# Kernel optimization log

Measured on AMD Instinct MI355X. Metric: run time of the kernel, lower is better.

The kernel has to match this reference:

```python
import jax, jax.numpy as jnp
import numpy as np

TAU = 2.0
V_TH = 1.0
ALPHA = 2.0  # ATan surrogate alpha (spikingjelly default)

@jax.custom_vjp
def atan_heaviside(x):
    # Forward: Heaviside spike; backward: ATan surrogate gradient.
    return (x >= 0).astype(x.dtype)

def _atan_fwd(x):
    return atan_heaviside(x), x

def _atan_bwd(x, g):
    sg = (ALPHA / 2.0) / (1.0 + (jnp.pi / 2.0 * ALPHA * x) ** 2)
    return (g * sg,)

atan_heaviside.defvjp(_atan_fwd, _atan_bwd)

def lif_scan(cur):
    # cur: [T, B, F] input currents. LIF: H = V + (X - V)/tau; S = H >= v_th; hard reset V = H*(1-S).
    def step(v, x_t):
        h = v + (x_t - v) / TAU
        s = atan_heaviside(h - V_TH)
        v_new = h * (1.0 - s)
        return v_new, s
    v0 = jnp.zeros(cur.shape[1:], dtype=cur.dtype)
    _, spikes = jax.lax.scan(step, v0, cur)
    return spikes

def setup_inputs() -> dict:
    key = jax.random.key(0)
    k1, k2 = jax.random.split(key)
    T, B, F_in, F_out = 64, 256, 1024, 1024
    x = jax.random.normal(k1, (T, B, F_in), dtype=jnp.float32)
    W = jax.random.normal(k2, (F_out, F_in), dtype=jnp.float32) * (1.0 / np.sqrt(F_in))
    return {"x": x, "W": W}

def reference(x, W):
    # Linear projection over all timesteps, then multi-step LIF recurrence.
    cur = jnp.einsum('tbf,of->tbo', x, W)  # [T, B, F_out]
    return lif_scan(cur)
```

## Files before the change

kernel.cpp:

```cpp
#include <hip/hip_runtime.h>


#define T_DIM 64
#define B_DIM 256
#define F_DIM 1024
#define K_DIM 1024
#define M_DIM 16384
#define COLS  (B_DIM * F_DIM)
#define KP    2048
#define MARGIN 6e-5f
#define LIST_CAP 32768

typedef __attribute__((ext_vector_type(8))) short short8;
typedef __attribute__((ext_vector_type(4))) float floatx4;

#define ASYNC_CP16(gp, lp)                                                     \
    __builtin_amdgcn_global_load_lds(                                          \
        (const __attribute__((address_space(1))) unsigned int*)(gp),           \
        (__attribute__((address_space(3))) unsigned int*)(lp), 16, 0, 0)

#define HARD_SYNC() do {                                                       \
        __builtin_amdgcn_sched_barrier(0);                                     \
        asm volatile("s_waitcnt vmcnt(0) lgkmcnt(0)" ::: "memory");            \
        __syncthreads();                                                       \
        __builtin_amdgcn_sched_barrier(0);                                     \
    } while (0)

__device__ inline unsigned short f32_to_bf16_rne(float f) {
    unsigned int u = __builtin_bit_cast(unsigned int, f);
    unsigned int r = (u + 0x7FFFu + ((u >> 16) & 1u)) >> 16;
    return (unsigned short)r;
}
__device__ inline float bf16_to_f32(unsigned short h) {
    unsigned int u = ((unsigned int)h) << 16;
    return __builtin_bit_cast(float, u);
}

__global__ __launch_bounds__(256) void split_kernel(
    const float* __restrict__ x, const float* __restrict__ Wm,
    unsigned short* __restrict__ A, unsigned short* __restrict__ B,
    unsigned int* __restrict__ counter)
{
    if (blockIdx.x == 0 && threadIdx.x == 0) *counter = 0;
    const int blk = blockIdx.x;
    const float* in;
    unsigned short* dst;
    int g2;
    int orow;
    if (blk < 8192) {
        g2 = blk * 256 + threadIdx.x;
        int e = g2 * 8;
        int row = e >> 10;
        orow = ((row & 255) << 6) | (row >> 8);
        in = x; dst = A;
    } else {
        g2 = (blk - 8192) * 256 + threadIdx.x;
        int e = g2 * 8;
        orow = e >> 10;
        in = Wm; dst = B;
    }
    const int k = (g2 * 8) & 1023;
    float4 v0 = reinterpret_cast<const float4*>(in)[g2 * 2];
    float4 v1 = reinterpret_cast<const float4*>(in)[g2 * 2 + 1];
    float fs[8] = {v0.x, v0.y, v0.z, v0.w, v1.x, v1.y, v1.z, v1.w};
    short8 hv, lv;
#pragma unroll
    for (int i = 0; i < 8; ++i) {
        unsigned short h = f32_to_bf16_rne(fs[i]);
        unsigned short l = f32_to_bf16_rne(fs[i] - bf16_to_f32(h));
        hv[i] = (short)h;
        lv[i] = (short)l;
    }
    reinterpret_cast<short8*>(dst)[(size_t)orow * (KP / 8) + (k >> 3)] = hv;
    reinterpret_cast<short8*>(dst)[(size_t)orow * (KP / 8) + 128 + (k >> 3)] = lv;
}

__global__ __launch_bounds__(512, 2) void gemm_scan_kernel(
    const unsigned short* __restrict__ A,
    const unsigned short* __restrict__ B,
    float* __restrict__ out,
    unsigned int* __restrict__ counter, unsigned int* __restrict__ list)
{
    __shared__ unsigned short Ah0[256 * 32], Al0[256 * 32];
    __shared__ unsigned short Bh0[256 * 32], Bl0[256 * 32];
    __shared__ unsigned short Ah1[256 * 32], Al1[256 * 32];
    __shared__ unsigned short Bh1[256 * 32], Bl1[256 * 32];

    const int tid  = threadIdx.x;
    const int lane = tid & 63;
    const int wv   = tid >> 6;
    const int lid = blockIdx.x;
    const int mt  = ((lid & 7) << 3) | (lid >> 5);
    const int nt  = (lid >> 3) & 3;
    const int m0  = mt * 256;
    const int n0  = nt * 256;
    const int wm  = (wv & 1) * 128;
    const int wn  = (wv >> 1) * 64;

    floatx4 acc[8][4] = {};

    const int srow = tid >> 2;
    const int slin = (tid & 3) * 8;
    const int ssw  = (((tid & 3) ^ ((srow >> 1) & 3)) * 8);
    const int lrow = lane & 15;
    const int q    = lane >> 4;
    const int rsw  = (lrow >> 1) & 3;
    const int sl   = (q ^ rsw) * 8;

    const size_t RKP = (size_t)128 * KP;
    const unsigned short* ga_h = A + (size_t)(m0 + srow) * KP + ssw;
    const unsigned short* ga_l = ga_h + 1024;
    const unsigned short* gb_h = B + (size_t)(n0 + srow) * KP + ssw;
    const unsigned short* gb_l = gb_h + 1024;

    const int ldsA  = srow * 32 + slin;
    const int ldsA2 = (srow + 128) * 32 + slin;

    int aoff[8], boff[4];
#pragma unroll
    for (int i = 0; i < 8; ++i) aoff[i] = (wm + i * 16 + lrow) * 32 + sl;
#pragma unroll
    for (int j = 0; j < 4; ++j) boff[j] = (wn + j * 16 + lrow) * 32 + sl;

#define STAGE(AhB, AlB, BhB, BlB, kk) do {                                     \
        ASYNC_CP16(ga_h + (kk),       &AhB[ldsA]);                             \
        ASYNC_CP16(ga_h + RKP + (kk), &AhB[ldsA2]);                            \
        ASYNC_CP16(ga_l + (kk),       &AlB[ldsA]);                             \
        ASYNC_CP16(ga_l + RKP + (kk), &AlB[ldsA2]);                            \
        ASYNC_CP16(gb_h + (kk),       &BhB[ldsA]);                             \
        ASYNC_CP16(gb_h + RKP + (kk), &BhB[ldsA2]);                            \
        ASYNC_CP16(gb_l + (kk),       &BlB[ldsA]);                             \
        ASYNC_CP16(gb_l + RKP + (kk), &BlB[ldsA2]);                            \
    } while (0)

#define COMPUTE(AhB, AlB, BhB, BlB) do {                                       \
        short8 ah[8], al[8];                                                   \
        _Pragma("unroll")                                                      \
        for (int i = 0; i < 8; ++i) {                                          \
            ah[i] = *reinterpret_cast<const short8*>(&AhB[aoff[i]]);           \
            al[i] = *reinterpret_cast<const short8*>(&AlB[aoff[i]]);           \
        }                                                                      \
        _Pragma("unroll")                                                      \
        for (int jh = 0; jh < 2; ++jh) {                                       \
            short8 bh[2], bl[2];                                               \
            _Pragma("unroll")                                                  \
            for (int j2 = 0; j2 < 2; ++j2) {                                   \
                bh[j2] = *reinterpret_cast<const short8*>(&BhB[boff[jh * 2 + j2]]); \
                bl[j2] = *reinterpret_cast<const short8*>(&BlB[boff[jh * 2 + j2]]); \
            }                                                                  \
            __builtin_amdgcn_s_setprio(1);                                     \
            _Pragma("unroll")                                                  \
            for (int i = 0; i < 8; ++i)                                        \
                _Pragma("unroll")                                              \
                for (int j2 = 0; j2 < 2; ++j2)                                 \
                    acc[i][jh * 2 + j2] = __builtin_amdgcn_mfma_f32_16x16x32_bf16( \
                        ah[i], bh[j2], acc[i][jh * 2 + j2], 0, 0, 0);          \
            _Pragma("unroll")                                                  \
            for (int i = 0; i < 8; ++i)                                        \
                _Pragma("unroll")                                              \
                for (int j2 = 0; j2 < 2; ++j2)                                 \
                    acc[i][jh * 2 + j2] = __builtin_amdgcn_mfma_f32_16x16x32_bf16( \
                        al[i], bh[j2], acc[i][jh * 2 + j2], 0, 0, 0);          \
            _Pragma("unroll")                                                  \
            for (int i = 0; i < 8; ++i)                                        \
                _Pragma("unroll")                                              \
                for (int j2 = 0; j2 < 2; ++j2)                                 \
                    acc[i][jh * 2 + j2] = __builtin_amdgcn_mfma_f32_16x16x32_bf16( \
                        ah[i], bl[j2], acc[i][jh * 2 + j2], 0, 0, 0);          \
            __builtin_amdgcn_s_setprio(0);                                     \
        }                                                                      \
    } while (0)

    STAGE(Ah0, Al0, Bh0, Bl0, 0);
    HARD_SYNC();

#pragma unroll 1
    for (int kt = 0; kt < 32; kt += 2) {
        STAGE(Ah1, Al1, Bh1, Bl1, (kt + 1) * 32);
        COMPUTE(Ah0, Al0, Bh0, Bl0);
        HARD_SYNC();
        if (kt + 2 < 32) STAGE(Ah0, Al0, Bh0, Bl0, (kt + 2) * 32);
        COMPUTE(Ah1, Al1, Bh1, Bl1);
        HARD_SYNC();
    }

#undef STAGE
#undef COMPUTE

    const int col = lane & 15;
    const int b_base = mt * 4 + (wv & 1) * 2;

    unsigned int fmask = 0;
#pragma unroll
    for (int hb = 0; hb < 2; ++hb) {
#pragma unroll
        for (int j = 0; j < 4; ++j) {
            float v = 0.f;
            bool fl = false;
#pragma unroll
            for (int i4 = 0; i4 < 4; ++i4) {
                const int i = hb * 4 + i4;
#pragma unroll
                for (int qq = 0; qq < 4; ++qq) {
                    if (q == qq) {
#pragma unroll
                        for (int r = 0; r < 4; ++r) {
                            float cu = acc[i][j][r];
                            float hm = v + (cu - v) * 0.5f;
                            float d = hm - 1.0f;
                            bool sp = (d >= 0.f);
                            fl |= (fabsf(d) < MARGIN);
                            acc[i][j][r] = sp ? 1.0f : 0.0f;
                            v = sp ? 0.f : hm;
                        }
                    }
                    v = __shfl(v, qq * 16 + col, 64);
                }
            }
            if (fl) fmask |= (1u << (hb * 4 + j));
        }
    }
    fmask |= __shfl_xor(fmask, 16, 64);
    fmask |= __shfl_xor(fmask, 32, 64);

#pragma unroll
    for (int i = 0; i < 8; ++i) {
        float* outp = out + (size_t)(b_base + (i >> 2)) * F_DIM;
        const int tb = (i & 3) * 16 + q * 4;
#pragma unroll
        for (int j = 0; j < 4; ++j)
#pragma unroll
            for (int r = 0; r < 4; ++r)
                outp[(size_t)(tb + r) * COLS + (n0 + wn + j * 16 + col)] = acc[i][j][r];
    }

    if (q == 0 && fmask) {
        for (int hb = 0; hb < 2; ++hb)
            for (int j = 0; j < 4; ++j)
                if (fmask & (1u << (hb * 4 + j))) {
                    unsigned int idx = atomicAdd(counter, 1u);
                    if (idx < LIST_CAP)
                        list[idx] = (unsigned int)(((b_base + hb) << 10) |
                                                   (n0 + wn + j * 16 + col));
                }
    }
}

__global__ __launch_bounds__(256) void fixup_kernel(
    const float* __restrict__ x, const float* __restrict__ W,
    const unsigned int* __restrict__ counter, const unsigned int* __restrict__ list,
    float* __restrict__ out)
{
    __shared__ double curd[T_DIM];
    __shared__ float wrow[K_DIM];
    unsigned int n = *counter;
    if (n > LIST_CAP) n = LIST_CAP;
    const int wv = threadIdx.x >> 6, lane = threadIdx.x & 63;

    for (unsigned int idx = blockIdx.x; idx < n; idx += gridDim.x) {
        const unsigned int c = list[idx];
        const int b = c >> 10, o = c & 1023;
        __syncthreads();
        for (int k = threadIdx.x; k < K_DIM; k += 256) wrow[k] = W[(size_t)o * K_DIM + k];
        __syncthreads();
        for (int it = 0; it < 16; ++it) {
            const int t = it * 4 + wv;
            const float* xp = x + (size_t)t * COLS + (size_t)b * F_DIM + lane * 16;
            double s = 0.0;
#pragma unroll
            for (int qq = 0; qq < 4; ++qq) {
                float4 xv = reinterpret_cast<const float4*>(xp)[qq];
                float4 wq = *reinterpret_cast<const float4*>(&wrow[lane * 16 + qq * 4]);
                s += (double)xv.x * (double)wq.x + (double)xv.y * (double)wq.y +
                     (double)xv.z * (double)wq.z + (double)xv.w * (double)wq.w;
            }
#pragma unroll
            for (int off = 32; off > 0; off >>= 1) s += __shfl_down(s, off, 64);
            if (lane == 0) curd[t] = s;
        }
        __syncthreads();
        if (threadIdx.x == 0) {
            double v = 0.0;
            for (int t = 0; t < T_DIM; ++t) {
                double h = v + (curd[t] - v) * 0.5;
                bool s = (h >= 1.0);
                out[(size_t)t * COLS + c] = s ? 1.0f : 0.0f;
                v = s ? 0.0 : h;
            }
        }
        __syncthreads();
    }
}

#define TILE 64
#define KC 32
#define XS_LD 36
#define SC_LD 65

__global__ __launch_bounds__(256) void lif_fused_kernel(
    const float* __restrict__ x, const float* __restrict__ Wm, float* __restrict__ out)
{
    __shared__ __align__(16) unsigned char smem_raw[TILE * SC_LD * sizeof(double)];
    float* sf = reinterpret_cast<float*>(smem_raw);
    double* sd = reinterpret_cast<double*>(smem_raw);
    float* Xs = sf;
    float* Ws = sf + TILE * XS_LD;

    const int b = blockIdx.y;
    const int o0 = blockIdx.x * TILE;
    const int tid = threadIdx.x;
    const int tx = tid & 15, ty = tid >> 4;

    double acc[4][4];
#pragma unroll
    for (int i = 0; i < 4; ++i)
#pragma unroll
        for (int j = 0; j < 4; ++j) acc[i][j] = 0.0;

    const int r = tid >> 3, c4 = (tid & 7) * 4;
    const float* xbase = x + (size_t)b * F_DIM;

    for (int k0 = 0; k0 < K_DIM; k0 += KC) {
        __syncthreads();
        float4 xv0 = *reinterpret_cast<const float4*>(xbase + (size_t)r * COLS + k0 + c4);
        float4 xv1 = *reinterpret_cast<const float4*>(xbase + (size_t)(r + 32) * COLS + k0 + c4);
        *reinterpret_cast<float4*>(Xs + r * XS_LD + c4) = xv0;
        *reinterpret_cast<float4*>(Xs + (r + 32) * XS_LD + c4) = xv1;
        float4 wv0 = *reinterpret_cast<const float4*>(Wm + (size_t)(o0 + r) * K_DIM + k0 + c4);
        float4 wv1 = *reinterpret_cast<const float4*>(Wm + (size_t)(o0 + r + 32) * K_DIM + k0 + c4);
        *reinterpret_cast<float4*>(Ws + r * XS_LD + c4) = wv0;
        *reinterpret_cast<float4*>(Ws + (r + 32) * XS_LD + c4) = wv1;
        __syncthreads();
#pragma unroll 4
        for (int kk = 0; kk < KC; ++kk) {
            double xa[4], wb[4];
#pragma unroll
            for (int i = 0; i < 4; ++i) xa[i] = (double)Xs[(4 * ty + i) * XS_LD + kk];
#pragma unroll
            for (int j = 0; j < 4; ++j) wb[j] = (double)Ws[(4 * tx + j) * XS_LD + kk];
#pragma unroll
            for (int i = 0; i < 4; ++i)
#pragma unroll
                for (int j = 0; j < 4; ++j) acc[i][j] = fma(xa[i], wb[j], acc[i][j]);
        }
    }
    __syncthreads();
#pragma unroll
    for (int i = 0; i < 4; ++i)
#pragma unroll
        for (int j = 0; j < 4; ++j) sd[(4 * ty + i) * SC_LD + (4 * tx + j)] = acc[i][j];
    __syncthreads();
    if (tid < TILE) {
        double v = 0.0;
        float* outp = out + (size_t)b * F_DIM + o0 + tid;
        for (int t = 0; t < T_DIM; ++t) {
            double cu = sd[t * SC_LD + tid];
            double h = v + (cu - v) * 0.5;
            bool s = (h >= 1.0);
            outp[(size_t)t * COLS] = s ? 1.0f : 0.0f;
            v = s ? 0.0 : h;
        }
    }
}

extern "C" void kernel_launch(void* const* d_in, const int* in_sizes, int n_in,
                              void* d_out, int out_size, void* d_ws, size_t ws_size,
                              hipStream_t stream) {
    const float* x = (const float*)d_in[0];
    const float* Wm = (const float*)d_in[1];
    float* out = (float*)d_out;

    const size_t OFF_A   = 0;
    const size_t OFF_B   = OFF_A + (size_t)M_DIM * KP * 2;
    const size_t OFF_CNT = OFF_B + (size_t)F_DIM * KP * 2;
    const size_t OFF_LST = OFF_CNT + 256;
    const size_t NEEDED  = OFF_LST + (size_t)LIST_CAP * 4;

    if (ws_size < NEEDED) {
        dim3 grid(F_DIM / TILE, B_DIM, 1);
        lif_fused_kernel<<<grid, dim3(256), 0, stream>>>(x, Wm, out);
        return;
    }

    unsigned char* ws = (unsigned char*)d_ws;
    unsigned short* Abuf = (unsigned short*)(ws + OFF_A);
    unsigned short* Bbuf = (unsigned short*)(ws + OFF_B);
    unsigned int* counter = (unsigned int*)(ws + OFF_CNT);
    unsigned int* list = (unsigned int*)(ws + OFF_LST);

    split_kernel<<<dim3(8192 + 512), dim3(256), 0, stream>>>(x, Wm, Abuf, Bbuf, counter);
    gemm_scan_kernel<<<dim3(256), dim3(512), 0, stream>>>(Abuf, Bbuf, out, counter, list);
    fixup_kernel<<<dim3(512), dim3(256), 0, stream>>>(x, Wm, counter, list, out);
}
```

Measured before the change: 223.9 us.

## Fuse x bf16 hi/lo split into GEMM A-tile staging, drop A workspace

The separate pre-pass that split x into bf16 high/low halves and wrote a permuted 64 MB A buffer is removed. The GEMM kernel now loads fp32 x directly into registers, converts it to hi/lo bf16 and writes both halves to LDS, overlapping the global loads with the previous tile's MFMA compute. This removes a full read and write round trip of the A operand through global memory. In exchange it adds conversion ALU work and register pressure inside the GEMM loop, and the synchronous register loads replace async global-to-LDS copies.

```diff
diff --git a/kernel.cpp b/kernel.cpp
--- a/kernel.cpp
+++ b/kernel.cpp
@@ -36,32 +36,17 @@
     return __builtin_bit_cast(float, u);
 }
 
-__global__ __launch_bounds__(256) void split_kernel(
-    const float* __restrict__ x, const float* __restrict__ Wm,
-    unsigned short* __restrict__ A, unsigned short* __restrict__ B,
+__global__ __launch_bounds__(256) void split_w_kernel(
+    const float* __restrict__ Wm, unsigned short* __restrict__ B,
     unsigned int* __restrict__ counter)
 {
     if (blockIdx.x == 0 && threadIdx.x == 0) *counter = 0;
-    const int blk = blockIdx.x;
-    const float* in;
-    unsigned short* dst;
-    int g2;
-    int orow;
-    if (blk < 8192) {
-        g2 = blk * 256 + threadIdx.x;
-        int e = g2 * 8;
-        int row = e >> 10;
-        orow = ((row & 255) << 6) | (row >> 8);
-        in = x; dst = A;
-    } else {
-        g2 = (blk - 8192) * 256 + threadIdx.x;
-        int e = g2 * 8;
-        orow = e >> 10;
-        in = Wm; dst = B;
-    }
-    const int k = (g2 * 8) & 1023;
-    float4 v0 = reinterpret_cast<const float4*>(in)[g2 * 2];
-    float4 v1 = reinterpret_cast<const float4*>(in)[g2 * 2 + 1];
+    const int g2 = blockIdx.x * 256 + threadIdx.x;
+    const int e = g2 * 8;
+    const int orow = e >> 10;
+    const int k = e & 1023;
+    float4 v0 = reinterpret_cast<const float4*>(Wm)[g2 * 2];
+    float4 v1 = reinterpret_cast<const float4*>(Wm)[g2 * 2 + 1];
     float fs[8] = {v0.x, v0.y, v0.z, v0.w, v1.x, v1.y, v1.z, v1.w};
     short8 hv, lv;
 #pragma unroll
@@ -71,12 +56,12 @@
         hv[i] = (short)h;
         lv[i] = (short)l;
     }
-    reinterpret_cast<short8*>(dst)[(size_t)orow * (KP / 8) + (k >> 3)] = hv;
-    reinterpret_cast<short8*>(dst)[(size_t)orow * (KP / 8) + 128 + (k >> 3)] = lv;
+    reinterpret_cast<short8*>(B)[(size_t)orow * (KP / 8) + (k >> 3)] = hv;
+    reinterpret_cast<short8*>(B)[(size_t)orow * (KP / 8) + 128 + (k >> 3)] = lv;
 }
 
 __global__ __launch_bounds__(512, 2) void gemm_scan_kernel(
-    const unsigned short* __restrict__ A,
+    const float* __restrict__ x,
     const unsigned short* __restrict__ B,
     float* __restrict__ out,
     unsigned int* __restrict__ counter, unsigned int* __restrict__ list)
@@ -107,9 +92,14 @@
     const int rsw  = (lrow >> 1) & 3;
     const int sl   = (q ^ rsw) * 8;
 
+    const int ar0 = m0 + srow;
+    const int ar1 = ar0 + 128;
+    const float* xr0 =
+        x + ((size_t)(ar0 & 63) * 256 + (ar0 >> 6)) * 1024 + ssw;
+    const float* xr1 =
+        x + ((size_t)(ar1 & 63) * 256 + (ar1 >> 6)) * 1024 + ssw;
+
     const size_t RKP = (size_t)128 * KP;
-    const unsigned short* ga_h = A + (size_t)(m0 + srow) * KP + ssw;
-    const unsigned short* ga_l = ga_h + 1024;
     const unsigned short* gb_h = B + (size_t)(n0 + srow) * KP + ssw;
     const unsigned short* gb_l = gb_h + 1024;
 
@@ -122,15 +112,39 @@
 #pragma unroll
     for (int j = 0; j < 4; ++j) boff[j] = (wn + j * 16 + lrow) * 32 + sl;
 
-#define STAGE(AhB, AlB, BhB, BlB, kk) do {                                     \
-        ASYNC_CP16(ga_h + (kk),       &AhB[ldsA]);                             \
-        ASYNC_CP16(ga_h + RKP + (kk), &AhB[ldsA2]);                            \
-        ASYNC_CP16(ga_l + (kk),       &AlB[ldsA]);                             \
-        ASYNC_CP16(ga_l + RKP + (kk), &AlB[ldsA2]);                            \
+    float4 fA0, fA0b, fA1, fA1b;
+
+#define STAGE_A_LOAD(kk) do {                                                  \
+        fA0  = *reinterpret_cast<const float4*>(xr0 + (kk));                   \
+        fA0b = *reinterpret_cast<const float4*>(xr0 + (kk) + 4);               \
+        fA1  = *reinterpret_cast<const float4*>(xr1 + (kk));                   \
+        fA1b = *reinterpret_cast<const float4*>(xr1 + (kk) + 4);               \
+    } while (0)
+
+#define STAGE_B(BhB, BlB, kk) do {                                             \
         ASYNC_CP16(gb_h + (kk),       &BhB[ldsA]);                             \
         ASYNC_CP16(gb_h + RKP + (kk), &BhB[ldsA2]);                            \
         ASYNC_CP16(gb_l + (kk),       &BlB[ldsA]);                             \
         ASYNC_CP16(gb_l + RKP + (kk), &BlB[ldsA2]);                            \
+    } while (0)
+
+#define CVT8(dsth, dstl, va, vb) do {                                          \
+        float fs[8] = {va.x, va.y, va.z, va.w, vb.x, vb.y, vb.z, vb.w};        \
+        short8 hv, lv;                                                         \
+        _Pragma("unroll")                                                      \
+        for (int ii = 0; ii < 8; ++ii) {                                       \
+            unsigned short h = f32_to_bf16_rne(fs[ii]);                        \
+            unsigned short l = f32_to_bf16_rne(fs[ii] - bf16_to_f32(h));       \
+            hv[ii] = (short)h;                                                 \
+            lv[ii] = (short)l;                                                 \
+        }                                                                      \
+        *reinterpret_cast<short8*>(dsth) = hv;                                 \
+        *reinterpret_cast<short8*>(dstl) = lv;                                 \
+    } while (0)
+
+#define CVT_WRITE(AhB, AlB) do {                                               \
+        CVT8(&AhB[ldsA],  &AlB[ldsA],  fA0, fA0b);                             \
+        CVT8(&AhB[ldsA2], &AlB[ldsA2], fA1, fA1b);                             \
     } while (0)
 
 #define COMPUTE(AhB, AlB, BhB, BlB) do {                                       \
@@ -171,20 +185,35 @@
         }                                                                      \
     } while (0)
 
-    STAGE(Ah0, Al0, Bh0, Bl0, 0);
+    STAGE_A_LOAD(0);
+    STAGE_B(Bh0, Bl0, 0);
+    CVT_WRITE(Ah0, Al0);
     HARD_SYNC();
 
 #pragma unroll 1
     for (int kt = 0; kt < 32; kt += 2) {
-        STAGE(Ah1, Al1, Bh1, Bl1, (kt + 1) * 32);
+        STAGE_A_LOAD((kt + 1) * 32);
+        STAGE_B(Bh1, Bl1, (kt + 1) * 32);
+        __builtin_amdgcn_sched_barrier(0);
         COMPUTE(Ah0, Al0, Bh0, Bl0);
+        __builtin_amdgcn_sched_barrier(0);
+        CVT_WRITE(Ah1, Al1);
         HARD_SYNC();
-        if (kt + 2 < 32) STAGE(Ah0, Al0, Bh0, Bl0, (kt + 2) * 32);
+        if (kt + 2 < 32) {
+            STAGE_A_LOAD((kt + 2) * 32);
+            STAGE_B(Bh0, Bl0, (kt + 2) * 32);
+        }
+        __builtin_amdgcn_sched_barrier(0);
         COMPUTE(Ah1, Al1, Bh1, Bl1);
+        __builtin_amdgcn_sched_barrier(0);
+        if (kt + 2 < 32) CVT_WRITE(Ah0, Al0);
         HARD_SYNC();
     }
 
-#undef STAGE
+#undef STAGE_A_LOAD
+#undef STAGE_B
+#undef CVT8
+#undef CVT_WRITE
 #undef COMPUTE
 
     const int col = lane & 15;
@@ -370,8 +399,7 @@
     const float* Wm = (const float*)d_in[1];
     float* out = (float*)d_out;
 
-    const size_t OFF_A   = 0;
-    const size_t OFF_B   = OFF_A + (size_t)M_DIM * KP * 2;
+    const size_t OFF_B   = 0;
     const size_t OFF_CNT = OFF_B + (size_t)F_DIM * KP * 2;
     const size_t OFF_LST = OFF_CNT + 256;
     const size_t NEEDED  = OFF_LST + (size_t)LIST_CAP * 4;
@@ -383,12 +411,11 @@
     }
 
     unsigned char* ws = (unsigned char*)d_ws;
-    unsigned short* Abuf = (unsigned short*)(ws + OFF_A);
     unsigned short* Bbuf = (unsigned short*)(ws + OFF_B);
     unsigned int* counter = (unsigned int*)(ws + OFF_CNT);
     unsigned int* list = (unsigned int*)(ws + OFF_LST);
 
-    split_kernel<<<dim3(8192 + 512), dim3(256), 0, stream>>>(x, Wm, Abuf, Bbuf, counter);
-    gemm_scan_kernel<<<dim3(256), dim3(512), 0, stream>>>(Abuf, Bbuf, out, counter, list);
+    split_w_kernel<<<dim3(512), dim3(256), 0, stream>>>(Wm, Bbuf, counter);
+    gemm_scan_kernel<<<dim3(256), dim3(512), 0, stream>>>(x, Bbuf, out, counter, list);
     fixup_kernel<<<dim3(512), dim3(256), 0, stream>>>(x, Wm, counter, list, out);
 }
```

Result: slower. 240.7 us (+7.5%).
